# Optimization experiments

Measured on AMD Instinct MI355X. Metric: run time of the kernel, lower is better.

Reference implementation:

```python
import jax, jax.numpy as jnp
import numpy as np

VOCAB = 50257
EXTRA = 64          # static over-approximation of num_oovs
SEQ = 1024
T_DEC = 100
E = 128
H = 160             # encoder hidden per direction; decoder hidden = 2H = 320
UNK = 3
START = 0
NEG = -1e9


def lstm_cell(x, h, c, wih, whh, bih, bhh):
    # torch gate order: i, f, g, o
    g = x @ wih.T + h @ whh.T + bih + bhh
    i, f, gg, o = jnp.split(g, 4, axis=-1)
    c = jax.nn.sigmoid(f) * c + jax.nn.sigmoid(i) * jnp.tanh(gg)
    h = jax.nn.sigmoid(o) * jnp.tanh(c)
    return h, c


def run_lstm(xs, wih, whh, bih, bhh, hdim):
    def step(carry, x):
        h, c = carry
        h, c = lstm_cell(x, h, c, wih, whh, bih, bhh)
        return (h, c), h
    init = (jnp.zeros((hdim,), xs.dtype), jnp.zeros((hdim,), xs.dtype))
    (hf, _), hs = jax.lax.scan(step, init, xs)
    return hs, hf


def setup_inputs() -> dict:
    key = jax.random.key(0)
    ks = jax.random.split(key, 20)
    rn = lambda k, shape, s: (jax.random.normal(k, shape, dtype=jnp.float32) * s)
    inp = {
        'input_ids': jax.random.randint(ks[0], (SEQ,), 0, VOCAB + EXTRA),
        'embedding': rn(ks[1], (VOCAB, E), 0.1),
        'enc_wih_f': rn(ks[2], (4 * H, E), 0.08),
        'enc_whh_f': rn(ks[3], (4 * H, H), 0.08),
        'enc_bih_f': rn(ks[4], (4 * H,), 0.05),
        'enc_bhh_f': rn(ks[5], (4 * H,), 0.05),
        'enc_wih_b': rn(ks[6], (4 * H, E), 0.08),
        'enc_whh_b': rn(ks[7], (4 * H, H), 0.08),
        'enc_bih_b': rn(ks[8], (4 * H,), 0.05),
        'enc_bhh_b': rn(ks[9], (4 * H,), 0.05),
        'dec_wih': rn(ks[10], (8 * H, E), 0.08),
        'dec_whh': rn(ks[11], (8 * H, 2 * H), 0.08),
        'dec_bih': rn(ks[12], (8 * H,), 0.05),
        'dec_bhh': rn(ks[13], (8 * H,), 0.05),
        'enc_attn_proj': rn(ks[14], (2 * H, 2 * H), 0.02),
        'dec_attn_proj': rn(ks[15], (2 * H, 2 * H), 0.02),
        'vocab_proj': rn(ks[16], (E, 6 * H), 0.05),
        'out_bias': rn(ks[17], (VOCAB,), 0.01),
        'switch_w': rn(ks[18], (1, 6 * H), 0.05),
        'switch_b': rn(ks[19], (1,), 0.05),
    }
    return inp


def reference(input_ids, embedding, enc_wih_f, enc_whh_f, enc_bih_f, enc_bhh_f,
              enc_wih_b, enc_whh_b, enc_bih_b, enc_bhh_b,
              dec_wih, dec_whh, dec_bih, dec_bhh,
              enc_attn_proj, dec_attn_proj, vocab_proj, out_bias,
              switch_w, switch_b):
    ids_in = jnp.where(input_ids >= VOCAB, UNK, input_ids)
    emb = embedding[ids_in]                               # [S, E]

    # bidirectional encoder LSTM
    h_fwd, hfin_f = run_lstm(emb, enc_wih_f, enc_whh_f, enc_bih_f, enc_bhh_f, H)
    h_bwd_rev, hfin_b = run_lstm(emb[::-1], enc_wih_b, enc_whh_b, enc_bih_b, enc_bhh_b, H)
    enc_h = jnp.concatenate([h_fwd, h_bwd_rev[::-1]], axis=-1)   # [S, 2H]

    # step-invariant vocab projection: tanh(W_emb @ vocab_proj) -> [V, 6H]
    out_proj = jnp.tanh(embedding @ vocab_proj)

    # precompute projected encoder states for attention: [S, 2H]
    enc_proj_h = enc_h @ enc_attn_proj.T

    h0 = jnp.concatenate([hfin_f, hfin_b])                # [2H]
    c0 = jnp.zeros((2 * H,), enc_h.dtype)
    dec_buf0 = jnp.zeros((T_DEC, 2 * H), enc_h.dtype)
    cum0 = jnp.zeros((SEQ,), enc_h.dtype)
    tok0 = jnp.asarray(START, dtype=input_ids.dtype)
    t_range = jnp.arange(T_DEC)

    def step(carry, t):
        h, c, cum, dec_buf, tok = carry
        x = embedding[jnp.where(tok >= VOCAB, UNK, tok)]
        h, c = lstm_cell(x, h, c, dec_wih, dec_whh, dec_bih, dec_bhh)

        # intra-temporal encoder attention
        scores = enc_proj_h @ h                           # [S] = h @ W_e @ enc_h.T
        cum_safe = jnp.where(t == 0, 1.0, cum)
        temporal = jnp.where(t == 0, scores, jnp.exp(scores) / cum_safe)
        attn = jax.nn.softmax(temporal)
        enc_ctx = attn @ enc_h                            # [2H]

        # intra-decoder attention over previous decoder hidden states
        dscores = (h @ dec_attn_proj) @ dec_buf.T         # [T_DEC]
        dmask = t_range < t
        dattn = jax.nn.softmax(jnp.where(dmask, dscores, NEG))
        dec_ctx = jnp.where(t == 0, jnp.zeros_like(h), dattn @ dec_buf)

        concat = jnp.concatenate([h, enc_ctx, dec_ctx])   # [6H]
        vocab_dist = jax.nn.softmax(out_proj @ concat + out_bias)  # [V]
        p_copy = jax.nn.sigmoid(jnp.dot(switch_w[0], concat) + switch_b[0])
        gen = jnp.pad((1.0 - p_copy) * vocab_dist, (0, EXTRA))     # [V+EXTRA]
        final = gen.at[input_ids].add(p_copy * attn)      # pointer scatter-add

        cum = cum + scores
        dec_buf = dec_buf.at[t].set(h)
        tok = jnp.argmax(final).astype(input_ids.dtype)   # greedy decode
        return (h, c, cum, dec_buf, tok), final

    _, finals = jax.lax.scan(step, (h0, c0, cum0, dec_buf0, tok0), t_range)
    return finals                                         # [T_DEC, V+EXTRA]
```

## Files before the change

kernel.cpp:

```cpp
#include <hip/hip_runtime.h>
#include <cstdint>

#define VOCAB 50257
#define VTOT  50321
#define TDEC  100
#define UNK   3
#define NBLK  256
#define NTHR  512
#define VPB   198

static const size_t OFF_EMB    = 0;
static const size_t OFF_WIHT_F = 131072;
static const size_t OFF_WIHT_B = 212992;
static const size_t OFF_WTE    = 294912;
static const size_t OFF_XG     = 397312;
static const size_t OFF_ENCH   = 1708032;
static const size_t OFF_EPH    = 2035712;
static const size_t OFF_DECBUF = 2363392;
static const size_t OFF_LOGITS = 2395392;
static const size_t OFF_SCORES = 2446080;
static const size_t OFF_GATES  = 2447104;
static const size_t OFF_HPAR   = 2448384;
static const size_t OFF_CPAR   = 2450944;
static const size_t OFF_DCTX   = 2456064;
static const size_t OFF_H      = 2456384;
static const size_t OFF_H0     = 2456704;
static const size_t OFF_CA     = 2457024;
static const size_t OFF_CB     = 2457344;
static const size_t OFF_CUMA   = 2457664;
static const size_t OFF_CUMB   = 2458688;
static const size_t OFF_ATTN   = 2459712;
static const size_t OFF_BM     = 2460736;
static const size_t OFF_BS     = 2461248;
static const size_t OFF_AVAL   = 2461760;
static const size_t OFF_AIDX   = 2462272;
static const size_t OFF_SCAL   = 2462784;
static const size_t OFF_SKEY   = 2462848;
static const size_t OFF_SPOS   = 2463872;
static const size_t OFF_BSTART = 2464896;
static const size_t OFF_WBF16  = 2465792;

static const size_t OFF_PMS  = OFF_LOGITS;
static const size_t OFF_TEMP = OFF_SCORES;
static const size_t OFF_BAR  = OFF_SCAL;

__device__ __forceinline__ float sigmf(float x) { return 1.f / (1.f + expf(-x)); }

__device__ __forceinline__ float wsum64(float x) {
#pragma unroll
  for (int m = 1; m < 64; m <<= 1) x += __shfl_xor(x, m, 64);
  return x;
}

__device__ __forceinline__ unsigned short bf16r(float x) {
  uint32_t b = __float_as_uint(x);
  uint32_t r = (b + 0x7fffu + ((b >> 16) & 1u)) >> 16;
  return (unsigned short)r;
}

__device__ __forceinline__ float cload(const float* p) {
  return __hip_atomic_load((float*)p, __ATOMIC_RELAXED, __HIP_MEMORY_SCOPE_AGENT);
}
__device__ __forceinline__ void cstore(float* p, float v) {
  __hip_atomic_store(p, v, __ATOMIC_RELAXED, __HIP_MEMORY_SCOPE_AGENT);
}
__device__ __forceinline__ int cloadi(const int* p) {
  return __hip_atomic_load((int*)p, __ATOMIC_RELAXED, __HIP_MEMORY_SCOPE_AGENT);
}
__device__ __forceinline__ void cstorei(int* p, int v) {
  __hip_atomic_store(p, v, __ATOMIC_RELAXED, __HIP_MEMORY_SCOPE_AGENT);
}

__device__ __forceinline__ void gridbar(float* ws) {
  int* bar = (int*)(ws + OFF_BAR);
  __syncthreads();
  if (threadIdx.x == 0) {
    asm volatile("s_waitcnt vmcnt(0) lgkmcnt(0)" ::: "memory");
    int g = __hip_atomic_load(&bar[32], __ATOMIC_RELAXED, __HIP_MEMORY_SCOPE_AGENT);
    int old = __hip_atomic_fetch_add(&bar[0], 1, __ATOMIC_RELAXED, __HIP_MEMORY_SCOPE_AGENT);
    if (old == NBLK - 1) {
      __hip_atomic_store(&bar[0], 0, __ATOMIC_RELAXED, __HIP_MEMORY_SCOPE_AGENT);
      __hip_atomic_store(&bar[32], g + 1, __ATOMIC_RELAXED, __HIP_MEMORY_SCOPE_AGENT);
    } else {
      while (__hip_atomic_load(&bar[32], __ATOMIC_RELAXED, __HIP_MEMORY_SCOPE_AGENT) == g)
        __builtin_amdgcn_s_sleep(2);
    }
  }
  __syncthreads();
}

__global__ __launch_bounds__(256) void k_setup(float* __restrict__ ws, const int* __restrict__ ids,
                                               const float* __restrict__ embt, const float* __restrict__ ewf,
                                               const float* __restrict__ ewb, const float* __restrict__ eap) {
  int idx = blockIdx.x * 256 + threadIdx.x;
  if (idx < 131072) {
    int tt = idx >> 7, e = idx & 127;
    int id = ids[tt]; if (id >= VOCAB) id = UNK;
    ws[OFF_EMB + idx] = embt[(size_t)id * 128 + e];
  } else if (idx < 212992) {
    int i = idx - 131072;
    int k = i / 640, g = i - (i / 640) * 640;
    ws[OFF_WIHT_F + i] = ewf[(size_t)g * 128 + k];
  } else if (idx < 294912) {
    int i = idx - 212992;
    int k = i / 640, g = i - (i / 640) * 640;
    ws[OFF_WIHT_B + i] = ewb[(size_t)g * 128 + k];
  } else if (idx < 397312) {
    int i = idx - 294912;
    int k = i / 320, j = i - (i / 320) * 320;
    ws[OFF_WTE + i] = eap[(size_t)j * 320 + k];
  }
}

__global__ __launch_bounds__(256) void k_xg(float* __restrict__ ws,
                                            const float* __restrict__ bif, const float* __restrict__ bhf,
                                            const float* __restrict__ bib, const float* __restrict__ bhb) {
  int idx = blockIdx.x * 256 + threadIdx.x;
  int d = idx / 655360;
  int r = idx - d * 655360;
  int tt = r / 640, g = r - (r / 640) * 640;
  const float* wT = ws + (d ? OFF_WIHT_B : OFF_WIHT_F);
  const float* er = ws + OFF_EMB + (size_t)(d ? (1023 - tt) : tt) * 128;
  float acc = d ? (bib[g] + bhb[g]) : (bif[g] + bhf[g]);
#pragma unroll 4
  for (int k = 0; k < 128; ++k) acc += er[k] * wT[(size_t)k * 640 + g];
  ws[OFF_XG + idx] = acc;
}

__global__ __launch_bounds__(256) void k_outproj(const float* __restrict__ embt, const float* __restrict__ vp,
                                                 float* __restrict__ ws) {
  __shared__ float As[64][128];
  __shared__ float Bs[128][64];
  const int tid = threadIdx.x;
  const int v0 = blockIdx.x * 64, n0 = blockIdx.y * 64;
  for (int c = 0; c < 32; ++c) {
    int idx = c * 256 + tid;
    int m = idx >> 7, k = idx & 127;
    int v = v0 + m;
    As[m][k] = (v < VOCAB) ? embt[(size_t)v * 128 + k] : 0.f;
    int k2 = idx >> 6, n = idx & 63;
    Bs[k2][n] = vp[(size_t)k2 * 960 + n0 + n];
  }
  __syncthreads();
  const int mi = tid >> 4, ni = tid & 15;
  float acc[4][4] = {};
  for (int k = 0; k < 128; ++k) {
    float a0 = As[mi * 4 + 0][k], a1 = As[mi * 4 + 1][k], a2 = As[mi * 4 + 2][k], a3 = As[mi * 4 + 3][k];
    float4 b = *(const float4*)&Bs[k][ni * 4];
    acc[0][0] += a0 * b.x; acc[0][1] += a0 * b.y; acc[0][2] += a0 * b.z; acc[0][3] += a0 * b.w;
    acc[1][0] += a1 * b.x; acc[1][1] += a1 * b.y; acc[1][2] += a1 * b.z; acc[1][3] += a1 * b.w;
    acc[2][0] += a2 * b.x; acc[2][1] += a2 * b.y; acc[2][2] += a2 * b.z; acc[2][3] += a2 * b.w;
    acc[3][0] += a3 * b.x; acc[3][1] += a3 * b.y; acc[3][2] += a3 * b.z; acc[3][3] += a3 * b.w;
  }
  unsigned short* W = (unsigned short*)(ws + OFF_WBF16);
#pragma unroll
  for (int i = 0; i < 4; ++i) {
    int v = v0 + mi * 4 + i;
    if (v < VOCAB) {
      ushort4 pk;
      pk.x = bf16r(tanhf(acc[i][0]));
      pk.y = bf16r(tanhf(acc[i][1]));
      pk.z = bf16r(tanhf(acc[i][2]));
      pk.w = bf16r(tanhf(acc[i][3]));
      *(ushort4*)&W[(size_t)v * 960 + n0 + ni * 4] = pk;
    }
  }
}

__global__ __launch_bounds__(512) void k_encoder(float* __restrict__ ws, const float* __restrict__ whh_f,
                                                 const float* __restrict__ whh_b) {
  const int dir = blockIdx.x;
  const int tid = threadIdx.x;
  const float* whh = dir ? whh_b : whh_f;
  const float* xg = ws + OFF_XG + (size_t)dir * 655360;
  __shared__ float hbuf[160];
  __shared__ float part[4][640];
  const int q = tid & 127, kg = tid >> 7, ks = kg * 40;
  float w[5][40];
#pragma unroll
  for (int j = 0; j < 5; ++j)
#pragma unroll
    for (int i = 0; i < 40; ++i)
      w[j][i] = whh[(size_t)(5 * q + j) * 160 + ks + i];
  float cst = 0.f;
  if (tid < 160) hbuf[tid] = 0.f;
  __syncthreads();
  for (int t = 0; t < 1024; ++t) {
    float acc[5] = {0.f, 0.f, 0.f, 0.f, 0.f};
#pragma unroll
    for (int i4 = 0; i4 < 10; ++i4) {
      float4 h4 = *(const float4*)&hbuf[ks + i4 * 4];
#pragma unroll
      for (int j = 0; j < 5; ++j)
        acc[j] += w[j][i4 * 4 + 0] * h4.x + w[j][i4 * 4 + 1] * h4.y + w[j][i4 * 4 + 2] * h4.z + w[j][i4 * 4 + 3] * h4.w;
    }
#pragma unroll
    for (int j = 0; j < 5; ++j) part[kg][5 * q + j] = acc[j];
    __syncthreads();
    if (tid < 160) {
      float gi = xg[(size_t)t * 640 + tid];
      float gf = xg[(size_t)t * 640 + 160 + tid];
      float gg = xg[(size_t)t * 640 + 320 + tid];
      float go = xg[(size_t)t * 640 + 480 + tid];
#pragma unroll
      for (int k2 = 0; k2 < 4; ++k2) {
        gi += part[k2][tid]; gf += part[k2][160 + tid];
        gg += part[k2][320 + tid]; go += part[k2][480 + tid];
      }
      cst = sigmf(gf) * cst + sigmf(gi) * tanhf(gg);
      float hn = sigmf(go) * tanhf(cst);
      hbuf[tid] = hn;
      int trow = dir ? (1023 - t) : t;
      ws[OFF_ENCH + (size_t)trow * 320 + dir * 160 + tid] = hn;
    }
    __syncthreads();
  }
  if (tid < 160) ws[OFF_H0 + dir * 160 + tid] = hbuf[tid];
}

__global__ __launch_bounds__(256) void k_encproj(float* __restrict__ ws) {
  int idx = blockIdx.x * 256 + threadIdx.x;
  int s = idx / 320, j = idx - (idx / 320) * 320;
  const float* er = ws + OFF_ENCH + (size_t)s * 320;
  const float* wt = ws + OFF_WTE;
  float acc = 0.f;
#pragma unroll 4
  for (int k = 0; k < 320; ++k) acc += er[k] * wt[(size_t)k * 320 + j];
  ws[OFF_EPH + idx] = acc;
}

__global__ __launch_bounds__(512) void k_sort(float* __restrict__ ws, const int* __restrict__ ids) {
  __shared__ int sk[1024], sp[1024];
  const int tid = threadIdx.x;
  for (int j = tid; j < 1024; j += 512) { sk[j] = ids[j]; sp[j] = j; }
  __syncthreads();
  for (int k = 2; k <= 1024; k <<= 1)
    for (int j = k >> 1; j > 0; j >>= 1) {
      for (int i = tid; i < 1024; i += 512) {
        int ixj = i ^ j;
        if (ixj > i) {
          bool up = ((i & k) == 0);
          int a = sk[i], b2 = sk[ixj];
          if (up ? (a > b2) : (a < b2)) {
            sk[i] = b2; sk[ixj] = a;
            int pa = sp[i]; sp[i] = sp[ixj]; sp[ixj] = pa;
          }
        }
      }
      __syncthreads();
    }
  int* BST = (int*)(ws + OFF_BSTART);
  int* SK = (int*)(ws + OFF_SKEY);
  int* SP = (int*)(ws + OFF_SPOS);
  for (int j = tid; j < 1024; j += 512) {
    SK[j] = sk[j]; SP[j] = sp[j];
    int o1 = sk[j] / VPB;
    int o0 = (j == 0) ? -1 : (sk[j - 1] / VPB);
    for (int o = o0 + 1; o <= o1; ++o) BST[o] = j;
  }
  if (tid == 0) {
    int olast = sk[1023] / VPB;
    for (int o = olast + 1; o <= NBLK; ++o) BST[o] = 1024;
    int* bar = (int*)(ws + OFF_BAR);
    bar[0] = 0; bar[32] = 0;
  }
}

__global__ __launch_bounds__(512) void k_decode(float* __restrict__ ws, float* __restrict__ out,
    const float* __restrict__ embt,
    const float* __restrict__ dwih, const float* __restrict__ dwhh,
    const float* __restrict__ dbih, const float* __restrict__ dbhh,
    const float* __restrict__ dap, const float* __restrict__ sw,
    const float* __restrict__ sb, const float* __restrict__ ob) {
  const int b = blockIdx.x, tid = threadIdx.x;
  const int l = tid & 63, w = tid >> 6;
  __shared__ float hL[320], cL[320];
  __shared__ __align__(16) float concatL[960];
  __shared__ float logitsL[VPB];
  __shared__ float tauL[4], cumL[4];
  __shared__ float redA[512], redB[512];
  __shared__ int   redI[512];
  __shared__ float attnL[64], dsL[128], daL[128], hpL[320];
  __shared__ float pcS;

  if (tid < 320) { hL[tid] = ws[OFF_H0 + tid]; cL[tid] = 0.f; }
  if (tid < 4) cumL[tid] = 0.f;
  __syncthreads();

  for (int t = 0; t < TDEC; ++t) {
    int token = 0;
    if (t > 0) {
      float av = -1e30f; int ai = 0;
      if (tid < 256) { av = cload(&ws[OFF_AVAL + tid]); ai = cloadi(((const int*)(ws + OFF_AIDX)) + tid); }
      redA[tid] = av; redI[tid] = ai;
      __syncthreads();
      for (int off = 256; off > 0; off >>= 1) {
        if (tid < off) {
          float v2 = redA[tid + off]; int i2 = redI[tid + off];
          if (v2 > redA[tid] || (v2 == redA[tid] && i2 < redI[tid])) { redA[tid] = v2; redI[tid] = i2; }
        }
        __syncthreads();
      }
      token = redI[0];
    }
    int tokm = (token >= VOCAB) ? UNK : token;
    if (w < 5) {
      const int r = 5 * b + w;
      float acc = dwih[(size_t)r * 128 + l] * embt[(size_t)tokm * 128 + l]
                + dwih[(size_t)r * 128 + 64 + l] * embt[(size_t)tokm * 128 + 64 + l];
#pragma unroll
      for (int c = 0; c < 5; ++c) acc += dwhh[(size_t)r * 320 + c * 64 + l] * hL[c * 64 + l];
      acc = wsum64(acc);
      if (l == 0) cstore(&ws[OFF_GATES + r], acc + dbih[r] + dbhh[r]);
    }
    gridbar(ws);

    if (tid < 320) {
      float gi = cload(&ws[OFF_GATES + tid]);
      float gf = cload(&ws[OFF_GATES + 320 + tid]);
      float gg = cload(&ws[OFF_GATES + 640 + tid]);
      float go = cload(&ws[OFF_GATES + 960 + tid]);
      float c = sigmf(gf) * cL[tid] + sigmf(gi) * tanhf(gg);
      cL[tid] = c;
      float hn = sigmf(go) * tanhf(c);
      hL[tid] = hn;
      if (b == 16) ws[OFF_DECBUF + (size_t)t * 320 + tid] = hn;
    }
    __syncthreads();
    if (w < 4) {
      const int srow = 4 * b + w;
      const float* er = ws + OFF_EPH + (size_t)srow * 320;
      float acc = 0.f;
#pragma unroll
      for (int c = 0; c < 5; ++c) acc += er[c * 64 + l] * hL[c * 64 + l];
      acc = wsum64(acc);
      float tau = (t == 0) ? acc : expf(acc) / cumL[w];
      if (l == 0) {
        tauL[w] = tau;
        cstore(&ws[OFF_TEMP + srow], tau);
        cumL[w] += acc;
      }
    }
    if (b < 8 && tid < 320) {
      float acc = 0.f;
#pragma unroll 8
      for (int ii = 0; ii < 40; ++ii) {
        int i = b * 40 + ii;
        acc += hL[i] * dap[(size_t)i * 320 + tid];
      }
      cstore(&ws[OFF_HPAR + b * 320 + tid], acc);
    }
    __syncthreads();
    if (tid == 0) {
      float m4 = fmaxf(fmaxf(tauL[0], tauL[1]), fmaxf(tauL[2], tauL[3]));
      float s4 = expf(tauL[0] - m4) + expf(tauL[1] - m4) + expf(tauL[2] - m4) + expf(tauL[3] - m4);
      cstore(&ws[OFF_PMS + 2 * b], m4);
      cstore(&ws[OFF_PMS + 2 * b + 1], s4);
    }
    gridbar(ws);

    if (b < 16) {
      float m = -1e30f, s = 0.f;
      if (tid < 256) { m = cload(&ws[OFF_PMS + 2 * tid]); s = cload(&ws[OFF_PMS + 2 * tid + 1]); }
      redA[tid] = m; redB[tid] = s;
      __syncthreads();
      for (int off = 256; off > 0; off >>= 1) {
        if (tid < off) {
          float m1 = redA[tid], m2 = redA[tid + off];
          float mx = fmaxf(m1, m2);
          redB[tid] = redB[tid] * expf(m1 - mx) + redB[tid + off] * expf(m2 - mx);
          redA[tid] = mx;
        }
        __syncthreads();
      }
      const float M = redA[0], S = redB[0];
      __syncthreads();
      if (tid < 64) {
        float a = expf(cload(&ws[OFF_TEMP + 64 * b + tid]) - M) / S;
        attnL[tid] = a;
        cstore(&ws[OFF_ATTN + 64 * b + tid], a);
      }
      __syncthreads();
      if (tid < 320) {
        float acc = 0.f;
        const float* eh = ws + OFF_ENCH + (size_t)(64 * b) * 320 + tid;
#pragma unroll 4
        for (int k2 = 0; k2 < 64; ++k2) acc += attnL[k2] * eh[(size_t)k2 * 320];
        cstore(&ws[OFF_CPAR + b * 320 + tid], acc);
      }
    } else if (b == 16) {
      if (tid < 320) {
        float a = 0.f;
#pragma unroll
        for (int q = 0; q < 8; ++q) a += cload(&ws[OFF_HPAR + q * 320 + tid]);
        hpL[tid] = a;
      }
      __syncthreads();
      float hpv[5];
#pragma unroll
      for (int c = 0; c < 5; ++c) hpv[c] = hpL[c * 64 + l];
#pragma unroll
      for (int k2 = 0; k2 < 13; ++k2) {
        int tp = w + 8 * k2;
        if (tp < t) {
          float acc = 0.f;
#pragma unroll
          for (int c = 0; c < 5; ++c) acc += hpv[c] * ws[OFF_DECBUF + (size_t)tp * 320 + c * 64 + l];
          acc = wsum64(acc);
          if (l == 0) dsL[tp] = acc;
        }
      }
      __syncthreads();
      float dv = -1e30f;
      if (tid < 128) { dv = (tid < t) ? dsL[tid] : -1e30f; redA[tid] = dv; }
      __syncthreads();
      for (int off = 64; off > 0; off >>= 1) { if (tid < off) redA[tid] = fmaxf(redA[tid], redA[tid + off]); __syncthreads(); }
      float dmx = redA[0];
      __syncthreads();
      float de = (tid < 128) ? expf(dv - dmx) : 0.f;
      if (tid < 128) redA[tid] = de;
      __syncthreads();
      for (int off = 64; off > 0; off >>= 1) { if (tid < off) redA[tid] += redA[tid + off]; __syncthreads(); }
      float dS = redA[0];
      __syncthreads();
      if (tid < 128) daL[tid] = de / dS;
      __syncthreads();
      if (tid < 320) {
        float acc = 0.f;
        for (int tp = 0; tp < t; ++tp) acc += daL[tp] * ws[OFF_DECBUF + (size_t)tp * 320 + tid];
        cstore(&ws[OFF_DCTX + tid], (t == 0) ? 0.f : acc);
      }
    }
    gridbar(ws);

    if (tid < 320) {
      float e = 0.f;
#pragma unroll
      for (int g2 = 0; g2 < 16; ++g2) e += cload(&ws[OFF_CPAR + g2 * 320 + tid]);
      concatL[tid] = hL[tid];
      concatL[320 + tid] = e;
      concatL[640 + tid] = cload(&ws[OFF_DCTX + tid]);
    }
    __syncthreads();
    if (w == 0) {
      float acc = 0.f;
#pragma unroll
      for (int c = 0; c < 15; ++c) acc += sw[c * 64 + l] * concatL[c * 64 + l];
      acc = wsum64(acc);
      if (l == 0) pcS = 1.f / (1.f + expf(-(acc + sb[0])));
    }
    {
      const unsigned* W = (const unsigned*)(ws + OFF_WBF16);
      const float2* cL2 = (const float2*)concatL;
      float cc0[7], cc1[7], ct0 = 0.f, ct1 = 0.f;
#pragma unroll
      for (int c = 0; c < 7; ++c) { float2 x = cL2[c * 64 + l]; cc0[c] = x.x; cc1[c] = x.y; }
      if (l < 32) { ct0 = concatL[896 + 2 * l]; ct1 = concatL[897 + 2 * l]; }
      const int vbase = b * VPB;
      const int r0 = w * 25, r1 = (w * 25 + 25 < VPB) ? (w * 25 + 25) : VPB;
      for (int r = r0; r < r1; r += 2) {
        int va = vbase + r, vb2 = va + 1;
        bool oka = (va < VOCAB);
        bool okb = (r + 1 < r1) && (vb2 < VOCAB);
        float acc0 = 0.f, acc1 = 0.f;
        const unsigned* rowa = W + (size_t)va * 480;
        const unsigned* rowb = W + (size_t)vb2 * 480;
        unsigned ua[7], ub[7], ta = 0, tb = 0;
        if (oka) {
#pragma unroll
          for (int c = 0; c < 7; ++c) ua[c] = rowa[c * 64 + l];
          if (l < 32) ta = rowa[448 + l];
        }
        if (okb) {
#pragma unroll
          for (int c = 0; c < 7; ++c) ub[c] = rowb[c * 64 + l];
          if (l < 32) tb = rowb[448 + l];
        }
        if (oka) {
#pragma unroll
          for (int c = 0; c < 7; ++c)
            acc0 += __uint_as_float(ua[c] << 16) * cc0[c] + __uint_as_float(ua[c] & 0xffff0000u) * cc1[c];
          if (l < 32) acc0 += __uint_as_float(ta << 16) * ct0 + __uint_as_float(ta & 0xffff0000u) * ct1;
        }
        if (okb) {
#pragma unroll
          for (int c = 0; c < 7; ++c)
            acc1 += __uint_as_float(ub[c] << 16) * cc0[c] + __uint_as_float(ub[c] & 0xffff0000u) * cc1[c];
          if (l < 32) acc1 += __uint_as_float(tb << 16) * ct0 + __uint_as_float(tb & 0xffff0000u) * ct1;
        }
        acc0 = wsum64(acc0);
        acc1 = wsum64(acc1);
        if (l == 0) {
          logitsL[r] = oka ? (acc0 + ob[va]) : -1e30f;
          if (r + 1 < r1) logitsL[r + 1] = okb ? (acc1 + ob[vb2]) : -1e30f;
        }
      }
    }
    __syncthreads();
    {
      float m = -1e30f, s = 0.f;
      if (tid < VPB) { float lv = logitsL[tid]; if (lv > -1e29f) { m = lv; s = 1.f; } }
      redA[tid] = m; redB[tid] = s;
      __syncthreads();
      for (int off = 256; off > 0; off >>= 1) {
        if (tid < off) {
          float m1 = redA[tid], m2 = redA[tid + off];
          float mx = fmaxf(m1, m2);
          redB[tid] = redB[tid] * expf(m1 - mx) + redB[tid + off] * expf(m2 - mx);
          redA[tid] = mx;
        }
        __syncthreads();
      }
      if (tid == 0) { cstore(&ws[OFF_BM + b], redA[0]); cstore(&ws[OFF_BS + b], redB[0]); }
    }
    gridbar(ws);

    {
      float m = -1e30f, s = 0.f;
      if (tid < 256) { m = cload(&ws[OFF_BM + tid]); s = cload(&ws[OFF_BS + tid]); }
      redA[tid] = m; redB[tid] = s;
      __syncthreads();
      for (int off = 256; off > 0; off >>= 1) {
        if (tid < off) {
          float m1 = redA[tid], m2 = redA[tid + off];
          float mx = fmaxf(m1, m2);
          redB[tid] = redB[tid] * expf(m1 - mx) + redB[tid + off] * expf(m2 - mx);
          redA[tid] = mx;
        }
        __syncthreads();
      }
      const float M = redA[0], Sg = redB[0];
      const float pc = pcS;
      const float scale = (1.f - pc) / Sg;
      __syncthreads();
      const int* BST = (const int*)(ws + OFF_BSTART);
      const int* SK = (const int*)(ws + OFF_SKEY);
      const int* SP = (const int*)(ws + OFF_SPOS);
      const int vbase = b * VPB;
      int v = vbase + tid;
      bool act = (tid < VPB) && (v < VTOT);
      float val = -1e30f;
      if (act) {
        val = (v < VOCAB) ? scale * expf(logitsL[tid] - M) : 0.f;
        int jb = BST[b], je = BST[b + 1];
        for (int j = jb; j < je; ++j)
          if (SK[j] == v) val += pc * cload(&ws[OFF_ATTN + SP[j]]);
        out[(size_t)t * VTOT + v] = val;
      }
      redA[tid] = act ? val : -1e30f; redI[tid] = v;
      __syncthreads();
      for (int off = 256; off > 0; off >>= 1) {
        if (tid < off) {
          float v2 = redA[tid + off]; int i2 = redI[tid + off];
          if (v2 > redA[tid] || (v2 == redA[tid] && i2 < redI[tid])) { redA[tid] = v2; redI[tid] = i2; }
        }
        __syncthreads();
      }
      if (tid == 0) { cstore(&ws[OFF_AVAL + b], redA[0]); cstorei(((int*)(ws + OFF_AIDX)) + b, redI[0]); }
    }
    gridbar(ws);
  }
}

extern "C" void kernel_launch(void* const* d_in, const int* in_sizes, int n_in,
                              void* d_out, int out_size, void* d_ws, size_t ws_size,
                              hipStream_t stream) {
  const int*   ids  = (const int*)d_in[0];
  const float* embt = (const float*)d_in[1];
  const float* ewf  = (const float*)d_in[2];
  const float* ehf  = (const float*)d_in[3];
  const float* ebif = (const float*)d_in[4];
  const float* ebhf = (const float*)d_in[5];
  const float* ewb  = (const float*)d_in[6];
  const float* ehb  = (const float*)d_in[7];
  const float* ebib = (const float*)d_in[8];
  const float* ebhb = (const float*)d_in[9];
  const float* dwih = (const float*)d_in[10];
  const float* dwhh = (const float*)d_in[11];
  const float* dbih = (const float*)d_in[12];
  const float* dbhh = (const float*)d_in[13];
  const float* eap  = (const float*)d_in[14];
  const float* dap  = (const float*)d_in[15];
  const float* vp   = (const float*)d_in[16];
  const float* ob   = (const float*)d_in[17];
  const float* sw   = (const float*)d_in[18];
  const float* sb   = (const float*)d_in[19];
  float* out = (float*)d_out;
  float* ws  = (float*)d_ws;

  k_setup<<<1558, 256, 0, stream>>>(ws, ids, embt, ewf, ewb, eap);
  k_xg<<<5120, 256, 0, stream>>>(ws, ebif, ebhf, ebib, ebhb);
  k_outproj<<<dim3(786, 15), 256, 0, stream>>>(embt, vp, ws);
  k_encoder<<<2, 512, 0, stream>>>(ws, ehf, ehb);
  k_encproj<<<1280, 256, 0, stream>>>(ws);
  k_sort<<<1, 512, 0, stream>>>(ws, ids);
  k_decode<<<NBLK, NTHR, 0, stream>>>(ws, out, embt, dwih, dwhh, dbih, dbhh, dap, sw, sb, ob);
}
```

Measured before the change: 7.094 ms.

## Transpose bf16 vocab weights and overlap h-part of logits with grid barrier

```diff
diff --git a/kernel.cpp b/kernel.cpp
--- a/kernel.cpp
+++ b/kernel.cpp
@@ -7,7 +7,8 @@
 #define UNK   3
 #define NBLK  256
 #define NTHR  512
-#define VPB   198
+#define VPB   256
+#define VPAD  50304
 
 static const size_t OFF_EMB    = 0;
 static const size_t OFF_WIHT_F = 131072;
@@ -17,32 +18,23 @@
 static const size_t OFF_ENCH   = 1708032;
 static const size_t OFF_EPH    = 2035712;
 static const size_t OFF_DECBUF = 2363392;
-static const size_t OFF_LOGITS = 2395392;
-static const size_t OFF_SCORES = 2446080;
-static const size_t OFF_GATES  = 2447104;
-static const size_t OFF_HPAR   = 2448384;
-static const size_t OFF_CPAR   = 2450944;
-static const size_t OFF_DCTX   = 2456064;
-static const size_t OFF_H      = 2456384;
-static const size_t OFF_H0     = 2456704;
-static const size_t OFF_CA     = 2457024;
-static const size_t OFF_CB     = 2457344;
-static const size_t OFF_CUMA   = 2457664;
-static const size_t OFF_CUMB   = 2458688;
-static const size_t OFF_ATTN   = 2459712;
-static const size_t OFF_BM     = 2460736;
-static const size_t OFF_BS     = 2461248;
-static const size_t OFF_AVAL   = 2461760;
-static const size_t OFF_AIDX   = 2462272;
-static const size_t OFF_SCAL   = 2462784;
-static const size_t OFF_SKEY   = 2462848;
-static const size_t OFF_SPOS   = 2463872;
-static const size_t OFF_BSTART = 2464896;
-static const size_t OFF_WBF16  = 2465792;
-
-static const size_t OFF_PMS  = OFF_LOGITS;
-static const size_t OFF_TEMP = OFF_SCORES;
-static const size_t OFF_BAR  = OFF_SCAL;
+static const size_t OFF_GATES  = 2395392;
+static const size_t OFF_HPAR   = 2396672;
+static const size_t OFF_CPAR   = 2399232;
+static const size_t OFF_DCTX   = 2404352;
+static const size_t OFF_H0     = 2404672;
+static const size_t OFF_TEMP   = 2404992;
+static const size_t OFF_ATTN   = 2406016;
+static const size_t OFF_PMS    = 2407040;
+static const size_t OFF_BM     = 2407552;
+static const size_t OFF_BS     = 2407808;
+static const size_t OFF_AVAL   = 2408064;
+static const size_t OFF_AIDX   = 2408320;
+static const size_t OFF_BAR    = 2408576;
+static const size_t OFF_SKEY   = 2408640;
+static const size_t OFF_SPOS   = 2409664;
+static const size_t OFF_BSTART = 2410688;
+static const size_t OFF_WT     = 2411008;
 
 __device__ __forceinline__ float sigmf(float x) { return 1.f / (1.f + expf(-x)); }
 
@@ -131,6 +123,7 @@
                                                  float* __restrict__ ws) {
   __shared__ float As[64][128];
   __shared__ float Bs[128][64];
+  __shared__ unsigned T[32][64];
   const int tid = threadIdx.x;
   const int v0 = blockIdx.x * 64, n0 = blockIdx.y * 64;
   for (int c = 0; c < 32; ++c) {
@@ -152,18 +145,22 @@
     acc[2][0] += a2 * b.x; acc[2][1] += a2 * b.y; acc[2][2] += a2 * b.z; acc[2][3] += a2 * b.w;
     acc[3][0] += a3 * b.x; acc[3][1] += a3 * b.y; acc[3][2] += a3 * b.z; acc[3][3] += a3 * b.w;
   }
-  unsigned short* W = (unsigned short*)(ws + OFF_WBF16);
 #pragma unroll
   for (int i = 0; i < 4; ++i) {
-    int v = v0 + mi * 4 + i;
-    if (v < VOCAB) {
-      ushort4 pk;
-      pk.x = bf16r(tanhf(acc[i][0]));
-      pk.y = bf16r(tanhf(acc[i][1]));
-      pk.z = bf16r(tanhf(acc[i][2]));
-      pk.w = bf16r(tanhf(acc[i][3]));
-      *(ushort4*)&W[(size_t)v * 960 + n0 + ni * 4] = pk;
-    }
+    unsigned p0 = (unsigned)bf16r(tanhf(acc[i][0])) | ((unsigned)bf16r(tanhf(acc[i][1])) << 16);
+    unsigned p1 = (unsigned)bf16r(tanhf(acc[i][2])) | ((unsigned)bf16r(tanhf(acc[i][3])) << 16);
+    T[2 * ni][mi * 4 + i] = p0;
+    T[2 * ni + 1][mi * 4 + i] = p1;
+  }
+  __syncthreads();
+  unsigned* WT = (unsigned*)(ws + OFF_WT);
+  const int kbase = n0 >> 1;
+#pragma unroll
+  for (int r = 0; r < 8; ++r) {
+    int idx = r * 256 + tid;
+    int fp = idx >> 6, col = idx & 63;
+    int v = v0 + col;
+    if (v < VOCAB) WT[(size_t)(kbase + fp) * VPAD + v] = T[fp][col];
   }
 }
 
@@ -274,7 +271,8 @@
     const float* __restrict__ sb, const float* __restrict__ ob) {
   const int b = blockIdx.x, tid = threadIdx.x;
   const int l = tid & 63, w = tid >> 6;
-  __shared__ float hL[320], cL[320];
+  __shared__ __align__(16) float hL[320];
+  __shared__ float cL[320];
   __shared__ __align__(16) float concatL[960];
   __shared__ float logitsL[VPB];
   __shared__ float tauL[4], cumL[4];
@@ -282,6 +280,10 @@
   __shared__ int   redI[512];
   __shared__ float attnL[64], dsL[128], daL[128], hpL[320];
   __shared__ float pcS;
+
+  const int vrow = b * VPB + (int)tid;
+  const bool myrow = (tid < VPB) && (vrow < VOCAB);
+  const unsigned* WT = (const unsigned*)(ws + OFF_WT);
 
   if (tid < 320) { hL[tid] = ws[OFF_H0 + tid]; cL[tid] = 0.f; }
   if (tid < 4) cumL[tid] = 0.f;
@@ -431,6 +433,17 @@
         cstore(&ws[OFF_DCTX + tid], (t == 0) ? 0.f : acc);
       }
     }
+    float ga0 = 0.f, ga1 = 0.f, ga2 = 0.f, ga3 = 0.f;
+    if (myrow) {
+      const unsigned* wp = WT + vrow;
+#pragma unroll 8
+      for (int k = 0; k < 160; ++k) {
+        unsigned u = wp[(size_t)k * VPAD];
+        float2 cv = *(const float2*)&hL[2 * k];
+        ga0 += __uint_as_float(u << 16) * cv.x;
+        ga1 += __uint_as_float(u & 0xffff0000u) * cv.y;
+      }
+    }
     gridbar(ws);
 
     if (tid < 320) {
@@ -449,53 +462,17 @@
       acc = wsum64(acc);
       if (l == 0) pcS = 1.f / (1.f + expf(-(acc + sb[0])));
     }
-    {
-      const unsigned* W = (const unsigned*)(ws + OFF_WBF16);
-      const float2* cL2 = (const float2*)concatL;
-      float cc0[7], cc1[7], ct0 = 0.f, ct1 = 0.f;
-#pragma unroll
-      for (int c = 0; c < 7; ++c) { float2 x = cL2[c * 64 + l]; cc0[c] = x.x; cc1[c] = x.y; }
-      if (l < 32) { ct0 = concatL[896 + 2 * l]; ct1 = concatL[897 + 2 * l]; }
-      const int vbase = b * VPB;
-      const int r0 = w * 25, r1 = (w * 25 + 25 < VPB) ? (w * 25 + 25) : VPB;
-      for (int r = r0; r < r1; r += 2) {
-        int va = vbase + r, vb2 = va + 1;
-        bool oka = (va < VOCAB);
-        bool okb = (r + 1 < r1) && (vb2 < VOCAB);
-        float acc0 = 0.f, acc1 = 0.f;
-        const unsigned* rowa = W + (size_t)va * 480;
-        const unsigned* rowb = W + (size_t)vb2 * 480;
-        unsigned ua[7], ub[7], ta = 0, tb = 0;
-        if (oka) {
-#pragma unroll
-          for (int c = 0; c < 7; ++c) ua[c] = rowa[c * 64 + l];
-          if (l < 32) ta = rowa[448 + l];
-        }
-        if (okb) {
-#pragma unroll
-          for (int c = 0; c < 7; ++c) ub[c] = rowb[c * 64 + l];
-          if (l < 32) tb = rowb[448 + l];
-        }
-        if (oka) {
-#pragma unroll
-          for (int c = 0; c < 7; ++c)
-            acc0 += __uint_as_float(ua[c] << 16) * cc0[c] + __uint_as_float(ua[c] & 0xffff0000u) * cc1[c];
-          if (l < 32) acc0 += __uint_as_float(ta << 16) * ct0 + __uint_as_float(ta & 0xffff0000u) * ct1;
-        }
-        if (okb) {
-#pragma unroll
-          for (int c = 0; c < 7; ++c)
-            acc1 += __uint_as_float(ub[c] << 16) * cc0[c] + __uint_as_float(ub[c] & 0xffff0000u) * cc1[c];
-          if (l < 32) acc1 += __uint_as_float(tb << 16) * ct0 + __uint_as_float(tb & 0xffff0000u) * ct1;
-        }
-        acc0 = wsum64(acc0);
-        acc1 = wsum64(acc1);
-        if (l == 0) {
-          logitsL[r] = oka ? (acc0 + ob[va]) : -1e30f;
-          if (r + 1 < r1) logitsL[r + 1] = okb ? (acc1 + ob[vb2]) : -1e30f;
-        }
-      }
-    }
+    if (myrow) {
+      const unsigned* wp = WT + vrow;
+#pragma unroll 8
+      for (int k = 160; k < 480; ++k) {
+        unsigned u = wp[(size_t)k * VPAD];
+        float2 cv = *(const float2*)&concatL[2 * k];
+        ga2 += __uint_as_float(u << 16) * cv.x;
+        ga3 += __uint_as_float(u & 0xffff0000u) * cv.y;
+      }
+    }
+    if (tid < VPB) logitsL[tid] = myrow ? (ga0 + ga1 + ga2 + ga3 + ob[vrow]) : -1e30f;
     __syncthreads();
     {
       float m = -1e30f, s = 0.f;
@@ -536,8 +513,7 @@
       const int* BST = (const int*)(ws + OFF_BSTART);
       const int* SK = (const int*)(ws + OFF_SKEY);
       const int* SP = (const int*)(ws + OFF_SPOS);
-      const int vbase = b * VPB;
-      int v = vbase + tid;
+      int v = b * VPB + (int)tid;
       bool act = (tid < VPB) && (v < VTOT);
       float val = -1e30f;
       if (act) {
```

New measurement: 8.833 ms. +24.5%, slower.

## Overlap h-part of vocab projection with attention phase, hierarchical grid barrier

Applied to the files above, without the earlier changes.

```diff
diff --git a/kernel.cpp b/kernel.cpp
--- a/kernel.cpp
+++ b/kernel.cpp
@@ -7,7 +7,9 @@
 #define UNK   3
 #define NBLK  256
 #define NTHR  512
-#define VPB   198
+#define NVA   150
+#define NVB   202
+#define SPLIT 2550
 
 static const size_t OFF_EMB    = 0;
 static const size_t OFF_WIHT_F = 131072;
@@ -17,33 +19,24 @@
 static const size_t OFF_ENCH   = 1708032;
 static const size_t OFF_EPH    = 2035712;
 static const size_t OFF_DECBUF = 2363392;
-static const size_t OFF_LOGITS = 2395392;
-static const size_t OFF_SCORES = 2446080;
-static const size_t OFF_GATES  = 2447104;
-static const size_t OFF_HPAR   = 2448384;
-static const size_t OFF_CPAR   = 2450944;
-static const size_t OFF_DCTX   = 2456064;
-static const size_t OFF_H      = 2456384;
-static const size_t OFF_H0     = 2456704;
-static const size_t OFF_CA     = 2457024;
-static const size_t OFF_CB     = 2457344;
-static const size_t OFF_CUMA   = 2457664;
-static const size_t OFF_CUMB   = 2458688;
+static const size_t OFF_GATES  = 2395392;
+static const size_t OFF_HPAR   = 2396672;
+static const size_t OFF_CPAR   = 2399232;
+static const size_t OFF_DCTX   = 2404352;
+static const size_t OFF_H0     = 2404672;
+static const size_t OFF_TEMP   = 2404992;
+static const size_t OFF_PMS    = 2406016;
 static const size_t OFF_ATTN   = 2459712;
 static const size_t OFF_BM     = 2460736;
 static const size_t OFF_BS     = 2461248;
 static const size_t OFF_AVAL   = 2461760;
 static const size_t OFF_AIDX   = 2462272;
-static const size_t OFF_SCAL   = 2462784;
+static const size_t OFF_BART   = 2457664;
 static const size_t OFF_SKEY   = 2462848;
 static const size_t OFF_SPOS   = 2463872;
 static const size_t OFF_BSTART = 2464896;
 static const size_t OFF_WBF16  = 2465792;
 
-static const size_t OFF_PMS  = OFF_LOGITS;
-static const size_t OFF_TEMP = OFF_SCORES;
-static const size_t OFF_BAR  = OFF_SCAL;
-
 __device__ __forceinline__ float sigmf(float x) { return 1.f / (1.f + expf(-x)); }
 
 __device__ __forceinline__ float wsum64(float x) {
@@ -58,6 +51,10 @@
   return (unsigned short)r;
 }
 
+__device__ __forceinline__ int vbmap(int v) {
+  return (v < SPLIT) ? (v / NVA) : (17 + (v - SPLIT) / NVB);
+}
+
 __device__ __forceinline__ float cload(const float* p) {
   return __hip_atomic_load((float*)p, __ATOMIC_RELAXED, __HIP_MEMORY_SCOPE_AGENT);
 }
@@ -71,20 +68,25 @@
   __hip_atomic_store(p, v, __ATOMIC_RELAXED, __HIP_MEMORY_SCOPE_AGENT);
 }
 
-__device__ __forceinline__ void gridbar(float* ws) {
-  int* bar = (int*)(ws + OFF_BAR);
+__device__ __forceinline__ void gridbar(float* ws, int b) {
+  int* bar = (int*)(ws + OFF_BART);
   __syncthreads();
   if (threadIdx.x == 0) {
     asm volatile("s_waitcnt vmcnt(0) lgkmcnt(0)" ::: "memory");
-    int g = __hip_atomic_load(&bar[32], __ATOMIC_RELAXED, __HIP_MEMORY_SCOPE_AGENT);
-    int old = __hip_atomic_fetch_add(&bar[0], 1, __ATOMIC_RELAXED, __HIP_MEMORY_SCOPE_AGENT);
-    if (old == NBLK - 1) {
-      __hip_atomic_store(&bar[0], 0, __ATOMIC_RELAXED, __HIP_MEMORY_SCOPE_AGENT);
-      __hip_atomic_store(&bar[32], g + 1, __ATOMIC_RELAXED, __HIP_MEMORY_SCOPE_AGENT);
-    } else {
-      while (__hip_atomic_load(&bar[32], __ATOMIC_RELAXED, __HIP_MEMORY_SCOPE_AGENT) == g)
-        __builtin_amdgcn_s_sleep(2);
-    }
+    const int g = b >> 4;
+    int* ggen = &bar[512 + g * 32];
+    int myg = __hip_atomic_load(ggen, __ATOMIC_RELAXED, __HIP_MEMORY_SCOPE_AGENT);
+    int old = __hip_atomic_fetch_add(&bar[g * 32], 1, __ATOMIC_RELAXED, __HIP_MEMORY_SCOPE_AGENT);
+    if ((old & 15) == 15) {
+      int r = __hip_atomic_fetch_add(&bar[1024], 1, __ATOMIC_RELAXED, __HIP_MEMORY_SCOPE_AGENT);
+      if ((r & 15) == 15) {
+#pragma unroll
+        for (int i = 0; i < 16; ++i)
+          __hip_atomic_store(&bar[512 + i * 32], myg + 1, __ATOMIC_RELAXED, __HIP_MEMORY_SCOPE_AGENT);
+      }
+    }
+    while (__hip_atomic_load(ggen, __ATOMIC_RELAXED, __HIP_MEMORY_SCOPE_AGENT) == myg)
+      __builtin_amdgcn_s_sleep(2);
   }
   __syncthreads();
 }
@@ -254,15 +256,20 @@
   int* SP = (int*)(ws + OFF_SPOS);
   for (int j = tid; j < 1024; j += 512) {
     SK[j] = sk[j]; SP[j] = sp[j];
-    int o1 = sk[j] / VPB;
-    int o0 = (j == 0) ? -1 : (sk[j - 1] / VPB);
+    int o1 = vbmap(sk[j]);
+    int o0 = (j == 0) ? -1 : vbmap(sk[j - 1]);
     for (int o = o0 + 1; o <= o1; ++o) BST[o] = j;
   }
+  for (int j = tid; j < 2048; j += 512) ((int*)(ws + OFF_BART))[j] = 0;
+  if (tid < 256) {
+    ws[OFF_AVAL + tid] = -1e30f;
+    ((int*)(ws + OFF_AIDX))[tid] = 0;
+    ws[OFF_BM + tid] = -1e30f;
+    ws[OFF_BS + tid] = 0.f;
+  }
   if (tid == 0) {
-    int olast = sk[1023] / VPB;
-    for (int o = olast + 1; o <= NBLK; ++o) BST[o] = 1024;
-    int* bar = (int*)(ws + OFF_BAR);
-    bar[0] = 0; bar[32] = 0;
+    int olast = vbmap(sk[1023]);
+    for (int o = olast + 1; o <= 256; ++o) BST[o] = 1024;
   }
 }
 
@@ -274,9 +281,17 @@
     const float* __restrict__ sb, const float* __restrict__ ob) {
   const int b = blockIdx.x, tid = threadIdx.x;
   const int l = tid & 63, w = tid >> 6;
-  __shared__ float hL[320], cL[320];
+  const int nv = (b < 17) ? NVA : NVB;
+  const int vbase = (b < 17) ? b * NVA : SPLIT + (b - 17) * NVB;
+  const bool hasout = vbase < VTOT;
+  const int rpw = (nv + 7) >> 3;
+  const int r0 = w * rpw, r1 = (r0 + rpw < nv) ? (r0 + rpw) : nv;
+
+  __shared__ __align__(16) float hL[320];
+  __shared__ float cL[320];
   __shared__ __align__(16) float concatL[960];
-  __shared__ float logitsL[VPB];
+  __shared__ float logitsL[204];
+  __shared__ float pCL[204];
   __shared__ float tauL[4], cumL[4];
   __shared__ float redA[512], redB[512];
   __shared__ int   redI[512];
@@ -286,6 +301,8 @@
   if (tid < 320) { hL[tid] = ws[OFF_H0 + tid]; cL[tid] = 0.f; }
   if (tid < 4) cumL[tid] = 0.f;
   __syncthreads();
+
+  const unsigned* W = (const unsigned*)(ws + OFF_WBF16);
 
   for (int t = 0; t < TDEC; ++t) {
     int token = 0;
@@ -313,7 +330,7 @@
       acc = wsum64(acc);
       if (l == 0) cstore(&ws[OFF_GATES + r], acc + dbih[r] + dbhh[r]);
     }
-    gridbar(ws);
+    gridbar(ws, b);
 
     if (tid < 320) {
       float gi = cload(&ws[OFF_GATES + tid]);
@@ -357,7 +374,7 @@
       cstore(&ws[OFF_PMS + 2 * b], m4);
       cstore(&ws[OFF_PMS + 2 * b + 1], s4);
     }
-    gridbar(ws);
+    gridbar(ws, b);
 
     if (b < 16) {
       float m = -1e30f, s = 0.f;
@@ -431,33 +448,11 @@
         cstore(&ws[OFF_DCTX + tid], (t == 0) ? 0.f : acc);
       }
     }
-    gridbar(ws);
-
-    if (tid < 320) {
-      float e = 0.f;
-#pragma unroll
-      for (int g2 = 0; g2 < 16; ++g2) e += cload(&ws[OFF_CPAR + g2 * 320 + tid]);
-      concatL[tid] = hL[tid];
-      concatL[320 + tid] = e;
-      concatL[640 + tid] = cload(&ws[OFF_DCTX + tid]);
-    }
-    __syncthreads();
-    if (w == 0) {
-      float acc = 0.f;
-#pragma unroll
-      for (int c = 0; c < 15; ++c) acc += sw[c * 64 + l] * concatL[c * 64 + l];
-      acc = wsum64(acc);
-      if (l == 0) pcS = 1.f / (1.f + expf(-(acc + sb[0])));
-    }
     {
-      const unsigned* W = (const unsigned*)(ws + OFF_WBF16);
-      const float2* cL2 = (const float2*)concatL;
-      float cc0[7], cc1[7], ct0 = 0.f, ct1 = 0.f;
-#pragma unroll
-      for (int c = 0; c < 7; ++c) { float2 x = cL2[c * 64 + l]; cc0[c] = x.x; cc1[c] = x.y; }
-      if (l < 32) { ct0 = concatL[896 + 2 * l]; ct1 = concatL[897 + 2 * l]; }
-      const int vbase = b * VPB;
-      const int r0 = w * 25, r1 = (w * 25 + 25 < VPB) ? (w * 25 + 25) : VPB;
+      const float2* hL2 = (const float2*)hL;
+      float hc0[2], hc1[2];
+#pragma unroll
+      for (int c = 0; c < 2; ++c) { float2 x = hL2[c * 64 + l]; hc0[c] = x.x; hc1[c] = x.y; }
       for (int r = r0; r < r1; r += 2) {
         int va = vbase + r, vb2 = va + 1;
         bool oka = (va < VOCAB);
@@ -465,41 +460,96 @@
         float acc0 = 0.f, acc1 = 0.f;
         const unsigned* rowa = W + (size_t)va * 480;
         const unsigned* rowb = W + (size_t)vb2 * 480;
-        unsigned ua[7], ub[7], ta = 0, tb = 0;
+        unsigned ua[2], ub[2];
+        if (oka) { ua[0] = rowa[l]; ua[1] = rowa[64 + l]; }
+        if (okb) { ub[0] = rowb[l]; ub[1] = rowb[64 + l]; }
         if (oka) {
 #pragma unroll
-          for (int c = 0; c < 7; ++c) ua[c] = rowa[c * 64 + l];
-          if (l < 32) ta = rowa[448 + l];
+          for (int c = 0; c < 2; ++c)
+            acc0 += __uint_as_float(ua[c] << 16) * hc0[c] + __uint_as_float(ua[c] & 0xffff0000u) * hc1[c];
         }
         if (okb) {
 #pragma unroll
-          for (int c = 0; c < 7; ++c) ub[c] = rowb[c * 64 + l];
-          if (l < 32) tb = rowb[448 + l];
-        }
-        if (oka) {
-#pragma unroll
-          for (int c = 0; c < 7; ++c)
-            acc0 += __uint_as_float(ua[c] << 16) * cc0[c] + __uint_as_float(ua[c] & 0xffff0000u) * cc1[c];
-          if (l < 32) acc0 += __uint_as_float(ta << 16) * ct0 + __uint_as_float(ta & 0xffff0000u) * ct1;
-        }
-        if (okb) {
-#pragma unroll
-          for (int c = 0; c < 7; ++c)
-            acc1 += __uint_as_float(ub[c] << 16) * cc0[c] + __uint_as_float(ub[c] & 0xffff0000u) * cc1[c];
-          if (l < 32) acc1 += __uint_as_float(tb << 16) * ct0 + __uint_as_float(tb & 0xffff0000u) * ct1;
+          for (int c = 0; c < 2; ++c)
+            acc1 += __uint_as_float(ub[c] << 16) * hc0[c] + __uint_as_float(ub[c] & 0xffff0000u) * hc1[c];
         }
         acc0 = wsum64(acc0);
         acc1 = wsum64(acc1);
         if (l == 0) {
-          logitsL[r] = oka ? (acc0 + ob[va]) : -1e30f;
-          if (r + 1 < r1) logitsL[r + 1] = okb ? (acc1 + ob[vb2]) : -1e30f;
+          pCL[r] = acc0;
+          if (r + 1 < r1) pCL[r + 1] = acc1;
+        }
+      }
+    }
+    gridbar(ws, b);
+
+    if (tid < 320) {
+      float e = 0.f;
+#pragma unroll
+      for (int g2 = 0; g2 < 16; ++g2) e += cload(&ws[OFF_CPAR + g2 * 320 + tid]);
+      concatL[tid] = hL[tid];
+      concatL[320 + tid] = e;
+      concatL[640 + tid] = cload(&ws[OFF_DCTX + tid]);
+    }
+    __syncthreads();
+    if (w == 0) {
+      float acc = 0.f;
+#pragma unroll
+      for (int c = 0; c < 15; ++c) acc += sw[c * 64 + l] * concatL[c * 64 + l];
+      acc = wsum64(acc);
+      if (l == 0) pcS = 1.f / (1.f + expf(-(acc + sb[0])));
+    }
+    {
+      const float2* cL2 = (const float2*)concatL;
+      float cc0[5], cc1[5], ct0 = 0.f, ct1 = 0.f;
+#pragma unroll
+      for (int c = 0; c < 5; ++c) { float2 x = cL2[(c + 2) * 64 + l]; cc0[c] = x.x; cc1[c] = x.y; }
+      if (l < 32) { ct0 = concatL[896 + 2 * l]; ct1 = concatL[897 + 2 * l]; }
+      for (int r = r0; r < r1; r += 2) {
+        int va = vbase + r, vb2 = va + 1;
+        bool oka = (va < VOCAB);
+        bool okb = (r + 1 < r1) && (vb2 < VOCAB);
+        float acc0 = 0.f, acc1 = 0.f;
+        const unsigned* rowa = W + (size_t)va * 480;
+        const unsigned* rowb = W + (size_t)vb2 * 480;
+        unsigned ua[5], ub[5], ta = 0, tb = 0;
+        if (oka) {
+#pragma unroll
+          for (int c = 0; c < 5; ++c) ua[c] = rowa[(c + 2) * 64 + l];
+          if (l < 32) ta = rowa[448 + l];
+        }
+        if (okb) {
+#pragma unroll
+          for (int c = 0; c < 5; ++c) ub[c] = rowb[(c + 2) * 64 + l];
+          if (l < 32) tb = rowb[448 + l];
+        }
+        if (oka) {
+#pragma unroll
+          for (int c = 0; c < 5; ++c)
+            acc0 += __uint_as_float(ua[c] << 16) * cc0[c] + __uint_as_float(ua[c] & 0xffff0000u) * cc1[c];
+          if (l < 32) acc0 += __uint_as_float(ta << 16) * ct0 + __uint_as_float(ta & 0xffff0000u) * ct1;
+        }
+        if (okb) {
+#pragma unroll
+          for (int c = 0; c < 5; ++c)
+            acc1 += __uint_as_float(ub[c] << 16) * cc0[c] + __uint_as_float(ub[c] & 0xffff0000u) * cc1[c];
+          if (l < 32) acc1 += __uint_as_float(tb << 16) * ct0 + __uint_as_float(tb & 0xffff0000u) * ct1;
+        }
+        acc0 = wsum64(acc0);
+        acc1 = wsum64(acc1);
+        if (l == 0) {
+          logitsL[r] = oka ? (pCL[r] + acc0 + ob[va]) : -1e30f;
+          if (r + 1 < r1) logitsL[r + 1] = okb ? (pCL[r + 1] + acc1 + ob[vb2]) : -1e30f;
         }
       }
     }
     __syncthreads();
     {
       float m = -1e30f, s = 0.f;
-      if (tid < VPB) { float lv = logitsL[tid]; if (lv > -1e29f) { m = lv; s = 1.f; } }
+      if (tid < nv) {
+        float lv = logitsL[tid];
+        if (lv > -1e29f) { m = lv; s = 1.f; }
+      }
       redA[tid] = m; redB[tid] = s;
       __syncthreads();
       for (int off = 256; off > 0; off >>= 1) {
@@ -511,9 +561,9 @@
         }
         __syncthreads();
       }
-      if (tid == 0) { cstore(&ws[OFF_BM + b], redA[0]); cstore(&ws[OFF_BS + b], redB[0]); }
-    }
-    gridbar(ws);
+      if (tid == 0 && hasout) { cstore(&ws[OFF_BM + b], redA[0]); cstore(&ws[OFF_BS + b], redB[0]); }
+    }
+    gridbar(ws, b);
 
     {
       float m = -1e30f, s = 0.f;
@@ -536,9 +586,8 @@
       const int* BST = (const int*)(ws + OFF_BSTART);
       const int* SK = (const int*)(ws + OFF_SKEY);
       const int* SP = (const int*)(ws + OFF_SPOS);
-      const int vbase = b * VPB;
       int v = vbase + tid;
-      bool act = (tid < VPB) && (v < VTOT);
+      bool act = (tid < nv) && (v < VTOT);
       float val = -1e30f;
       if (act) {
         val = (v < VOCAB) ? scale * expf(logitsL[tid] - M) : 0.f;
@@ -547,7 +596,7 @@
           if (SK[j] == v) val += pc * cload(&ws[OFF_ATTN + SP[j]]);
         out[(size_t)t * VTOT + v] = val;
       }
-      redA[tid] = act ? val : -1e30f; redI[tid] = v;
+      redA[tid] = act ? val : -1e30f; redI[tid] = act ? v : 0;
       __syncthreads();
       for (int off = 256; off > 0; off >>= 1) {
         if (tid < off) {
@@ -556,9 +605,9 @@
         }
         __syncthreads();
       }
-      if (tid == 0) { cstore(&ws[OFF_AVAL + b], redA[0]); cstorei(((int*)(ws + OFF_AIDX)) + b, redI[0]); }
-    }
-    gridbar(ws);
+      if (tid == 0 && hasout) { cstore(&ws[OFF_AVAL + b], redA[0]); cstorei(((int*)(ws + OFF_AIDX)) + b, redI[0]); }
+    }
+    gridbar(ws, b);
   }
 }
 
```

Result: slower. 10.19 ms (+43.6%).
